# Kernel optimization log

Hardware: AMD Instinct MI355X
Metric: run time of the kernel (lower is better)

The kernel has to match this reference:

```python
import jax, jax.numpy as jnp
import numpy as np

N = 50000   # nodes
R = 4       # relation groups
E = 800000  # nnz per relation adjacency
ED = 200000 # decoded edges
H = 128     # hidden_dim
L = 64      # latent_dim
DH = 64     # decoder_hidden_dim


def setup_inputs() -> dict:
    key = jax.random.key(0)
    ks = iter(jax.random.split(key, 64))
    def nrm(shape, scale=1.0):
        return jax.random.normal(next(ks), shape, dtype=jnp.float32) * scale
    inp = {}
    inp["x_process"] = nrm((N, 62))
    inp["x_file"] = nrm((N, 37))
    inp["x_network"] = nrm((N, 37))
    def lin(prefix, din, dout):
        s = 1.0 / np.sqrt(din)
        inp[prefix + "_Ws"] = nrm((dout, din), s)
        inp[prefix + "_bs"] = nrm((dout,), s)
        inp[prefix + "_Wr"] = nrm((R, dout, din), s)
        inp[prefix + "_br"] = nrm((R, dout), s)
    lin("p1", 62, H); lin("p2", H, L)
    lin("f1", 37, H); lin("f2", H, L)
    lin("n1", 37, H); lin("n2", H, L)
    inp["gate_W"] = nrm((3, L), 1.0 / np.sqrt(L))
    inp["gate_b"] = nrm((3,), 0.1)
    inp["dec_W1"] = nrm((DH, 4 * L), 1.0 / np.sqrt(4 * L))
    inp["dec_b1"] = nrm((DH,), 0.1)
    inp["dec_W2"] = nrm((1, DH), 1.0 / np.sqrt(DH))
    inp["dec_b2"] = nrm((1,), 0.1)
    inp["adj_rows"] = jax.random.randint(next(ks), (R, E), 0, N, dtype=jnp.int32)
    inp["adj_cols"] = jax.random.randint(next(ks), (R, E), 0, N, dtype=jnp.int32)
    inp["adj_vals"] = jax.random.uniform(next(ks), (R, E), dtype=jnp.float32) * 0.1
    inp["edge_src"] = jax.random.randint(next(ks), (ED,), 0, N, dtype=jnp.int32)
    inp["edge_dst"] = jax.random.randint(next(ks), (ED,), 0, N, dtype=jnp.int32)
    return inp


def reference(x_process, x_file, x_network,
              p1_Ws, p1_bs, p1_Wr, p1_br, p2_Ws, p2_bs, p2_Wr, p2_br,
              f1_Ws, f1_bs, f1_Wr, f1_br, f2_Ws, f2_bs, f2_Wr, f2_br,
              n1_Ws, n1_bs, n1_Wr, n1_br, n2_Ws, n2_bs, n2_Wr, n2_br,
              gate_W, gate_b, dec_W1, dec_b1, dec_W2, dec_b2,
              adj_rows, adj_cols, adj_vals, edge_src, edge_dst):
    def spmm(rows, cols, vals, x):  # A @ x, A in COO: out[row] += val * x[col]
        return jax.ops.segment_sum(vals[:, None] * x[cols], rows, num_segments=N)

    def rgcn_layer(x, Ws, bs, Wr, br):
        out = x @ Ws.T + bs  # self_linear
        for r in range(R):
            out = out + spmm(adj_rows[r], adj_cols[r], adj_vals[r], x) @ Wr[r].T + br[r]
        return out / float(R + 1)

    def encoder(x, W1s, b1s, W1r, b1r, W2s, b2s, W2r, b2r):
        h = jax.nn.relu(rgcn_layer(x, W1s, b1s, W1r, b1r))
        # dropout p=0.0 / eval mode -> identity
        return rgcn_layer(h, W2s, b2s, W2r, b2r)

    z_p = encoder(x_process, p1_Ws, p1_bs, p1_Wr, p1_br, p2_Ws, p2_bs, p2_Wr, p2_br)
    z_f = encoder(x_file, f1_Ws, f1_bs, f1_Wr, f1_br, f2_Ws, f2_bs, f2_Wr, f2_br)
    z_n = encoder(x_network, n1_Ws, n1_bs, n1_Wr, n1_br, n2_Ws, n2_bs, n2_Wr, n2_br)

    # gated multi-view fusion: three Linear(latent,1) gates -> softmax over views
    scores = jnp.stack([z_p @ gate_W[0] + gate_b[0],
                        z_f @ gate_W[1] + gate_b[1],
                        z_n @ gate_W[2] + gate_b[2]], axis=1)  # [N, 3]
    alpha = jax.nn.softmax(scores, axis=1)
    z = alpha[:, 0:1] * z_p + alpha[:, 1:2] * z_f + alpha[:, 2:3] * z_n  # [N, L]

    # mlp edge decoder
    zs = z[edge_src]
    zd = z[edge_dst]
    feats = jnp.concatenate([zs, zd, zs * zd, jnp.abs(zs - zd)], axis=1)  # [ED, 4L]
    hid = jax.nn.relu(feats @ dec_W1.T + dec_b1)
    logits = (hid @ dec_W2.T + dec_b2)[:, 0]  # [ED]
    return logits
```

## Files before the change

kernel.cpp:

```cpp
#include <hip/hip_runtime.h>

#define N_NODES 50000
#define R_REL   4
#define E_NNZ   800000
#define ED_EDGES 200000
#define H_DIM   128
#define L_DIM   64

#define RN_TOTAL (R_REL * N_NODES)
#define ETOT     (R_REL * E_NNZ)

#define EPB   8192
#define NB    391
#define RBK   196
#define KBK   (R_REL * RBK)
#define HTOT  (KBK * NB)
#define SCB   300
#define MAXB  6144

#define WS_RP    0u
#define WS_HIST  800256u
#define WS_BSUM  2026496u
#define WS_CV    2030592u
#define WS_TMP   27630720u
#define WS_XALL  53230720u
#define WS_SP    72430720u
#define WS_SF    122030720u
#define WS_SN    151630720u
#define WS_HPR   181230720u
#define WS_HN    WS_TMP
#define WS_HF    WS_SP
#define WS_YSP   WS_XALL
#define WS_YSF   (WS_SP + 25600000u)
#define WS_YRP   WS_SF
#define WS_YRF   WS_SN
#define WS_YSN   WS_HPR
#define WS_YRN   WS_HF
#define WS_Z     194030720u

__device__ __forceinline__ ushort f2bf(float f) {
    unsigned u = __float_as_uint(f);
    unsigned r = (u + 0x7fffu + ((u >> 16) & 1u)) >> 16;
    return (ushort)r;
}
__device__ __forceinline__ float bf2f(ushort u) {
    return __uint_as_float(((unsigned)u) << 16);
}

__global__ void cast_xall_kernel(const float* __restrict__ xp, const float* __restrict__ xf,
                                 const float* __restrict__ xn, ushort* __restrict__ xall) {
    int i = blockIdx.x * 256 + threadIdx.x;
    if (i >= N_NODES * 192) return;
    int node = i / 192, k = i - node * 192;
    float v = 0.f;
    if (k < 62) v = xp[node * 62 + k];
    else if (k >= 64 && k < 138) {
        int j = k - 64, d = j >> 1;
        v = (j & 1) ? xn[node * 37 + d] : xf[node * 37 + d];
    }
    xall[i] = f2bf(v);
}

__global__ void radix_hist_kernel(const int* __restrict__ rows, int* __restrict__ H) {
    __shared__ int hist[KBK];
    int blk = blockIdx.x, t = threadIdx.x;
    for (int i = t; i < KBK; i += 256) hist[i] = 0;
    __syncthreads();
    int base = blk * EPB;
    #pragma unroll 1
    for (int i = 0; i < EPB / 256; i++) {
        int g = base + i * 256 + t;
        if (g < ETOT) {
            int r = g / E_NNZ;
            atomicAdd(&hist[r * RBK + (rows[g] >> 8)], 1);
        }
    }
    __syncthreads();
    for (int i = t; i < KBK; i += 256) H[i * NB + blk] = hist[i];
}

__global__ void scan_part_kernel(const int* __restrict__ H, int* __restrict__ bsum) {
    __shared__ int red[256];
    int base = blockIdx.x * 1024, t = threadIdx.x;
    int s = 0;
    #pragma unroll
    for (int i = 0; i < 4; i++) {
        int idx = base + i * 256 + t;
        if (idx < HTOT) s += H[idx];
    }
    red[t] = s; __syncthreads();
    for (int d = 128; d > 0; d >>= 1) {
        if (t < d) red[t] += red[t + d];
        __syncthreads();
    }
    if (t == 0) bsum[blockIdx.x] = red[0];
}

__global__ void scan_bsum_kernel(int* __restrict__ bsum, int* __restrict__ rp) {
    __shared__ int sh[512];
    int t = threadIdx.x;
    int v = (t < SCB) ? bsum[t] : 0;
    sh[t] = v; __syncthreads();
    for (int d = 1; d < 512; d <<= 1) {
        int u = (t >= d) ? sh[t - d] : 0;
        __syncthreads();
        sh[t] += u;
        __syncthreads();
    }
    if (t < SCB) bsum[t] = sh[t] - v;
    if (t == 0) rp[RN_TOTAL] = ETOT;
}

__global__ void scan_final_kernel(int* __restrict__ H, const int* __restrict__ bsum) {
    __shared__ int sh[256];
    int base = blockIdx.x * 1024, t = threadIdx.x;
    int c[4]; int s = 0;
    #pragma unroll
    for (int i = 0; i < 4; i++) {
        int idx = base + t * 4 + i;
        c[i] = (idx < HTOT) ? H[idx] : 0;
        s += c[i];
    }
    sh[t] = s; __syncthreads();
    for (int d = 1; d < 256; d <<= 1) {
        int u = (t >= d) ? sh[t - d] : 0;
        __syncthreads();
        sh[t] += u;
        __syncthreads();
    }
    int off = bsum[blockIdx.x] + sh[t] - s;
    #pragma unroll
    for (int i = 0; i < 4; i++) {
        int idx = base + t * 4 + i;
        if (idx < HTOT) H[idx] = off;
        off += c[i];
    }
}

__global__ void radix_scatter_kernel(const int* __restrict__ rows, const int* __restrict__ cols,
                                     const float* __restrict__ vals, const int* __restrict__ H,
                                     int2* __restrict__ tmp) {
    __shared__ int cur[KBK];
    int blk = blockIdx.x, t = threadIdx.x;
    for (int i = t; i < KBK; i += 256) cur[i] = H[i * NB + blk];
    __syncthreads();
    int base = blk * EPB;
    #pragma unroll 1
    for (int i = 0; i < EPB / 256; i++) {
        int g = base + i * 256 + t;
        if (g < ETOT) {
            int r = g / E_NNZ;
            int row = rows[g];
            int b = r * RBK + (row >> 8);
            int p = atomicAdd(&cur[b], 1);
            tmp[p] = make_int2(cols[g] | ((row & 255) << 16), __float_as_int(vals[g]));
        }
    }
}

__launch_bounds__(256)
__global__ void bucket_sort_kernel(const int2* __restrict__ tmp, const int* __restrict__ H,
                                   int* __restrict__ rp, int2* __restrict__ cse) {
    __shared__ int hist[256];
    __shared__ int sc[256];
    __shared__ int cur[256];
    __shared__ int2 eb[MAXB];
    int b = blockIdx.x, t = threadIdx.x;
    int start = H[b * NB];
    int end = (b == KBK - 1) ? ETOT : H[(b + 1) * NB];
    int cnt = end - start;
    bool useLds = (cnt <= MAXB);
    hist[t] = 0;
    __syncthreads();
    for (int i = t; i < cnt; i += 256) {
        int2 e = tmp[start + i];
        if (useLds) eb[i] = e;
        atomicAdd(&hist[(e.x >> 16) & 255], 1);
    }
    __syncthreads();
    sc[t] = hist[t]; __syncthreads();
    for (int d = 1; d < 256; d <<= 1) {
        int v = (t >= d) ? sc[t - d] : 0;
        __syncthreads();
        sc[t] += v;
        __syncthreads();
    }
    int pref = sc[t] - hist[t];
    int r = b / RBK, rh = b - r * RBK;
    int grow = rh * 256 + t;
    if (grow < N_NODES) rp[r * N_NODES + grow] = start + pref;
    cur[t] = start + pref;
    __syncthreads();
    for (int i = t; i < cnt; i += 256) {
        int2 e = useLds ? eb[i] : tmp[start + i];
        int rl = (e.x >> 16) & 255;
        int p = atomicAdd(&cur[rl], 1);
        cse[p] = make_int2(e.x & 0xFFFF, e.y);
    }
}

__global__ void spmm1_all_kernel(const ushort* __restrict__ xall,
                                 const int* __restrict__ rp, const int2* __restrict__ cse,
                                 float* __restrict__ Sp, float* __restrict__ Sf,
                                 float* __restrict__ Sn) {
    int wave = threadIdx.x >> 6, lane = threadIdx.x & 63;
    int row = blockIdx.x * 4 + wave;
    if (row >= N_NODES) return;
    bool lp = lane < 62, lf = lane < 37;
    int opx = lane;
    int ofn = 64 + 2 * lane;
    for (int r = 0; r < R_REL; r++) {
        int e0 = rp[r * N_NODES + row], e1 = rp[r * N_NODES + row + 1];
        float ap = 0.f, af = 0.f, an = 0.f;
        int e = e0;
        for (; e + 4 <= e1; e += 4) {
            int2 q0 = cse[e], q1 = cse[e + 1], q2 = cse[e + 2], q3 = cse[e + 3];
            const ushort* b0 = xall + (size_t)q0.x * 192;
            const ushort* b1 = xall + (size_t)q1.x * 192;
            const ushort* b2 = xall + (size_t)q2.x * 192;
            const ushort* b3 = xall + (size_t)q3.x * 192;
            ushort  p0 = b0[opx], p1 = b1[opx], p2 = b2[opx], p3 = b3[opx];
            ushort2 u0 = *(const ushort2*)&b0[ofn];
            ushort2 u1 = *(const ushort2*)&b1[ofn];
            ushort2 u2 = *(const ushort2*)&b2[ofn];
            ushort2 u3 = *(const ushort2*)&b3[ofn];
            float v0 = __int_as_float(q0.y), v1 = __int_as_float(q1.y);
            float v2 = __int_as_float(q2.y), v3 = __int_as_float(q3.y);
            ap += v0 * bf2f(p0) + v1 * bf2f(p1) + v2 * bf2f(p2) + v3 * bf2f(p3);
            af += v0 * bf2f(u0.x) + v1 * bf2f(u1.x) + v2 * bf2f(u2.x) + v3 * bf2f(u3.x);
            an += v0 * bf2f(u0.y) + v1 * bf2f(u1.y) + v2 * bf2f(u2.y) + v3 * bf2f(u3.y);
        }
        for (; e < e1; e++) {
            int2 q = cse[e];
            const ushort* b = xall + (size_t)q.x * 192;
            float v = __int_as_float(q.y);
            ap += v * bf2f(b[opx]);
            ushort2 u = *(const ushort2*)&b[ofn];
            af += v * bf2f(u.x);
            an += v * bf2f(u.y);
        }
        if (lp) Sp[row * 248 + r * 62 + lane] = ap;
        if (lf) { Sf[row * 148 + r * 37 + lane] = af; Sn[row * 148 + r * 37 + lane] = an; }
    }
}

__launch_bounds__(256)
__global__ void gemm1_kernel(const float* __restrict__ x, const float* __restrict__ S,
                             const float* __restrict__ Ws, const float* __restrict__ bs,
                             const float* __restrict__ Wr, const float* __restrict__ br,
                             float* __restrict__ h, int din) {
    __shared__ float sA[64 * 63];
    __shared__ float sW[62 * 132];
    int t = threadIdx.x;
    int i0 = blockIdx.x * 64;
    int rg = t >> 5, cg = t & 31;
    float acc[8][4] = {};
    for (int s = 0; s < 5; s++) {
        const float* Aptr; int astride;
        if (s == 0) { Aptr = x; astride = din; }
        else        { Aptr = S + (s - 1) * din; astride = 4 * din; }
        const float* Wp = (s == 0) ? Ws : (Wr + (s - 1) * H_DIM * din);
        __syncthreads();
        for (int idx = t; idx < 64 * din; idx += 256) {
            int rr = idx / din, k = idx - rr * din;
            int grow = i0 + rr;
            sA[rr * 63 + k] = (grow < N_NODES) ? Aptr[grow * astride + k] : 0.f;
        }
        for (int idx = t; idx < H_DIM * din; idx += 256) {
            int j = idx / din, k = idx - j * din;
            sW[k * 132 + j] = Wp[j * din + k];
        }
        __syncthreads();
        for (int k = 0; k < din; k++) {
            float a[8];
            #pragma unroll
            for (int rr = 0; rr < 8; rr++) a[rr] = sA[(rg * 8 + rr) * 63 + k];
            float4 w = *(const float4*)&sW[k * 132 + cg * 4];
            #pragma unroll
            for (int rr = 0; rr < 8; rr++) {
                acc[rr][0] += a[rr] * w.x; acc[rr][1] += a[rr] * w.y;
                acc[rr][2] += a[rr] * w.z; acc[rr][3] += a[rr] * w.w;
            }
        }
    }
    int j0 = cg * 4;
    float btot[4];
    #pragma unroll
    for (int cc = 0; cc < 4; cc++) {
        float b = bs[j0 + cc];
        #pragma unroll
        for (int r = 0; r < R_REL; r++) b += br[r * H_DIM + j0 + cc];
        btot[cc] = b;
    }
    #pragma unroll
    for (int rr = 0; rr < 8; rr++) {
        int grow = i0 + rg * 8 + rr;
        if (grow < N_NODES) {
            float4 o;
            o.x = fmaxf((acc[rr][0] + btot[0]) * 0.2f, 0.f);
            o.y = fmaxf((acc[rr][1] + btot[1]) * 0.2f, 0.f);
            o.z = fmaxf((acc[rr][2] + btot[2]) * 0.2f, 0.f);
            o.w = fmaxf((acc[rr][3] + btot[3]) * 0.2f, 0.f);
            *(float4*)&h[grow * H_DIM + j0] = o;
        }
    }
}

__launch_bounds__(256)
__global__ void gemm2_kernel(const float* __restrict__ h, const float* __restrict__ Ws2,
                             const float* __restrict__ Wr2, float* __restrict__ Yself,
                             ushort* __restrict__ Yrel) {
    __shared__ float sA[128 * 65];
    __shared__ float sW[64 * 68];
    int t = threadIdx.x;
    int i0 = blockIdx.x * 128;
    int ct = blockIdx.y;
    int rg = t >> 4, cg = t & 15;
    const float* Wp = (ct == 0) ? Ws2 : (Wr2 + (ct - 1) * 64 * H_DIM);
    float acc[8][4] = {};
    for (int kc = 0; kc < 2; kc++) {
        __syncthreads();
        for (int idx = t; idx < 128 * 64; idx += 256) {
            int rr = idx >> 6, k = idx & 63;
            int grow = i0 + rr;
            sA[rr * 65 + k] = (grow < N_NODES) ? h[grow * H_DIM + kc * 64 + k] : 0.f;
        }
        for (int idx = t; idx < 64 * 64; idx += 256) {
            int j = idx >> 6, k = idx & 63;
            sW[k * 68 + j] = Wp[j * H_DIM + kc * 64 + k];
        }
        __syncthreads();
        for (int k = 0; k < 64; k++) {
            float a[8];
            #pragma unroll
            for (int rr = 0; rr < 8; rr++) a[rr] = sA[(rg * 8 + rr) * 65 + k];
            float4 w = *(const float4*)&sW[k * 68 + cg * 4];
            #pragma unroll
            for (int rr = 0; rr < 8; rr++) {
                acc[rr][0] += a[rr] * w.x; acc[rr][1] += a[rr] * w.y;
                acc[rr][2] += a[rr] * w.z; acc[rr][3] += a[rr] * w.w;
            }
        }
    }
    #pragma unroll
    for (int rr = 0; rr < 8; rr++) {
        int grow = i0 + rg * 8 + rr;
        if (grow < N_NODES) {
            if (ct == 0) {
                float4 o = make_float4(acc[rr][0], acc[rr][1], acc[rr][2], acc[rr][3]);
                *(float4*)&Yself[(size_t)grow * 64 + cg * 4] = o;
            } else {
                ushort4 o;
                o.x = f2bf(acc[rr][0]); o.y = f2bf(acc[rr][1]);
                o.z = f2bf(acc[rr][2]); o.w = f2bf(acc[rr][3]);
                *(ushort4*)&Yrel[(size_t)grow * 256 + (ct - 1) * 64 + cg * 4] = o;
            }
        }
    }
}

__global__ void spmm2z_all_kernel(const float* __restrict__ Ysp, const ushort* __restrict__ Yrp,
                                  const float* __restrict__ Ysf, const ushort* __restrict__ Yrf,
                                  const float* __restrict__ Ysn, const ushort* __restrict__ Yrn,
                                  const int* __restrict__ rp, const int2* __restrict__ cse,
                                  const float* __restrict__ p_bs, const float* __restrict__ p_br,
                                  const float* __restrict__ f_bs, const float* __restrict__ f_br,
                                  const float* __restrict__ n_bs, const float* __restrict__ n_br,
                                  const float* __restrict__ gW, const float* __restrict__ gb,
                                  float* __restrict__ z) {
    int wave = threadIdx.x >> 6, lane = threadIdx.x & 63;
    int row = blockIdx.x * 4 + wave;
    if (row >= N_NODES) return;
    float aP = Ysp[(size_t)row * 64 + lane] + p_bs[lane]
             + p_br[lane] + p_br[64 + lane] + p_br[128 + lane] + p_br[192 + lane];
    float aF = Ysf[(size_t)row * 64 + lane] + f_bs[lane]
             + f_br[lane] + f_br[64 + lane] + f_br[128 + lane] + f_br[192 + lane];
    float aN = Ysn[(size_t)row * 64 + lane] + n_bs[lane]
             + n_br[lane] + n_br[64 + lane] + n_br[128 + lane] + n_br[192 + lane];
    for (int r = 0; r < R_REL; r++) {
        int e0 = rp[r * N_NODES + row], e1 = rp[r * N_NODES + row + 1];
        const ushort* yp = Yrp + r * 64 + lane;
        const ushort* yf = Yrf + r * 64 + lane;
        const ushort* yn = Yrn + r * 64 + lane;
        int e = e0;
        for (; e + 4 <= e1; e += 4) {
            int2 q0 = cse[e], q1 = cse[e + 1], q2 = cse[e + 2], q3 = cse[e + 3];
            size_t o0 = (size_t)q0.x * 256, o1 = (size_t)q1.x * 256;
            size_t o2 = (size_t)q2.x * 256, o3 = (size_t)q3.x * 256;
            float pp0 = bf2f(yp[o0]), pp1 = bf2f(yp[o1]), pp2 = bf2f(yp[o2]), pp3 = bf2f(yp[o3]);
            float ff0 = bf2f(yf[o0]), ff1 = bf2f(yf[o1]), ff2 = bf2f(yf[o2]), ff3 = bf2f(yf[o3]);
            float nn0 = bf2f(yn[o0]), nn1 = bf2f(yn[o1]), nn2 = bf2f(yn[o2]), nn3 = bf2f(yn[o3]);
            float v0 = __int_as_float(q0.y), v1 = __int_as_float(q1.y);
            float v2 = __int_as_float(q2.y), v3 = __int_as_float(q3.y);
            aP += v0 * pp0 + v1 * pp1 + v2 * pp2 + v3 * pp3;
            aF += v0 * ff0 + v1 * ff1 + v2 * ff2 + v3 * ff3;
            aN += v0 * nn0 + v1 * nn1 + v2 * nn2 + v3 * nn3;
        }
        for (; e < e1; e++) {
            int2 q = cse[e];
            size_t o = (size_t)q.x * 256;
            float v = __int_as_float(q.y);
            aP += v * bf2f(yp[o]);
            aF += v * bf2f(yf[o]);
            aN += v * bf2f(yn[o]);
        }
    }
    aP *= 0.2f; aF *= 0.2f; aN *= 0.2f;
    float sp = aP * gW[lane], sf = aF * gW[64 + lane], sn = aN * gW[128 + lane];
    #pragma unroll
    for (int d = 32; d >= 1; d >>= 1) {
        sp += __shfl_xor(sp, d);
        sf += __shfl_xor(sf, d);
        sn += __shfl_xor(sn, d);
    }
    sp += gb[0]; sf += gb[1]; sn += gb[2];
    float m = fmaxf(sp, fmaxf(sf, sn));
    float ep = __expf(sp - m), ef = __expf(sf - m), en = __expf(sn - m);
    float inv = 1.f / (ep + ef + en);
    z[row * 64 + lane] = (ep * aP + ef * aF + en * aN) * inv;
}

__launch_bounds__(256)
__global__ void decoder4_kernel(const float* __restrict__ z, const int* __restrict__ esrc,
                                const int* __restrict__ edst, const float* __restrict__ w1,
                                const float* __restrict__ b1, const float* __restrict__ w2,
                                const float* __restrict__ b2, float* __restrict__ out) {
    __shared__ float sW1[16384];
    int t = threadIdx.x;
    for (int i = t; i < 4096; i += 256)
        ((float4*)sW1)[i] = ((const float4*)w1)[i];
    __syncthreads();
    int e1 = blockIdx.x * 512 + t;
    int e2 = e1 + 256;
    bool v2 = e2 < ED_EDGES;
    if (e1 >= ED_EDGES) return;
    int s1 = esrc[e1], d1 = edst[e1];
    int s2 = v2 ? esrc[e2] : s1;
    int d2 = v2 ? edst[e2] : d1;
    const float4* zs1 = (const float4*)(z + (size_t)s1 * 64);
    const float4* zd1 = (const float4*)(z + (size_t)d1 * 64);
    const float4* zs2 = (const float4*)(z + (size_t)s2 * 64);
    const float4* zd2 = (const float4*)(z + (size_t)d2 * 64);
    float hid1[64], hid2[64];
    #pragma unroll
    for (int j = 0; j < 64; j++) { hid1[j] = 0.f; hid2[j] = 0.f; }
    #pragma unroll 1
    for (int kc = 0; kc < 16; kc++) {
        float4 a1 = zs1[kc], b1v4 = zd1[kc];
        float4 a2 = zs2[kc], b2v4 = zd2[kc];
        float4 p1, q1, p2, q2;
        p1.x = a1.x * b1v4.x; q1.x = fabsf(a1.x - b1v4.x);
        p1.y = a1.y * b1v4.y; q1.y = fabsf(a1.y - b1v4.y);
        p1.z = a1.z * b1v4.z; q1.z = fabsf(a1.z - b1v4.z);
        p1.w = a1.w * b1v4.w; q1.w = fabsf(a1.w - b1v4.w);
        p2.x = a2.x * b2v4.x; q2.x = fabsf(a2.x - b2v4.x);
        p2.y = a2.y * b2v4.y; q2.y = fabsf(a2.y - b2v4.y);
        p2.z = a2.z * b2v4.z; q2.z = fabsf(a2.z - b2v4.z);
        p2.w = a2.w * b2v4.w; q2.w = fabsf(a2.w - b2v4.w);
        const float* wb0 = sW1 + kc * 4;
        #pragma unroll
        for (int j = 0; j < 64; j++) {
            const float* wr = wb0 + j * 256;
            float4 wa = *(const float4*)(wr);
            float4 wbv = *(const float4*)(wr + 64);
            float4 wc = *(const float4*)(wr + 128);
            float4 wd = *(const float4*)(wr + 192);
            hid1[j] += a1.x * wa.x + a1.y * wa.y + a1.z * wa.z + a1.w * wa.w
                     + b1v4.x * wbv.x + b1v4.y * wbv.y + b1v4.z * wbv.z + b1v4.w * wbv.w
                     + p1.x * wc.x + p1.y * wc.y + p1.z * wc.z + p1.w * wc.w
                     + q1.x * wd.x + q1.y * wd.y + q1.z * wd.z + q1.w * wd.w;
            hid2[j] += a2.x * wa.x + a2.y * wa.y + a2.z * wa.z + a2.w * wa.w
                     + b2v4.x * wbv.x + b2v4.y * wbv.y + b2v4.z * wbv.z + b2v4.w * wbv.w
                     + p2.x * wc.x + p2.y * wc.y + p2.z * wc.z + p2.w * wc.w
                     + q2.x * wd.x + q2.y * wd.y + q2.z * wd.z + q2.w * wd.w;
        }
    }
    float lg1 = b2[0], lg2 = b2[0];
    #pragma unroll
    for (int j = 0; j < 64; j++) {
        float bj = b1[j], wj = w2[j];
        lg1 += fmaxf(hid1[j] + bj, 0.f) * wj;
        lg2 += fmaxf(hid2[j] + bj, 0.f) * wj;
    }
    out[e1] = lg1;
    if (v2) out[e2] = lg2;
}

extern "C" void kernel_launch(void* const* d_in, const int* in_sizes, int n_in,
                              void* d_out, int out_size, void* d_ws, size_t ws_size,
                              hipStream_t stream) {
    const float* x_p = (const float*)d_in[0];
    const float* x_f = (const float*)d_in[1];
    const float* x_n = (const float*)d_in[2];
    const float* p1_Ws = (const float*)d_in[3];  const float* p1_bs = (const float*)d_in[4];
    const float* p1_Wr = (const float*)d_in[5];  const float* p1_br = (const float*)d_in[6];
    const float* p2_Ws = (const float*)d_in[7];  const float* p2_bs = (const float*)d_in[8];
    const float* p2_Wr = (const float*)d_in[9];  const float* p2_br = (const float*)d_in[10];
    const float* f1_Ws = (const float*)d_in[11]; const float* f1_bs = (const float*)d_in[12];
    const float* f1_Wr = (const float*)d_in[13]; const float* f1_br = (const float*)d_in[14];
    const float* f2_Ws = (const float*)d_in[15]; const float* f2_bs = (const float*)d_in[16];
    const float* f2_Wr = (const float*)d_in[17]; const float* f2_br = (const float*)d_in[18];
    const float* n1_Ws = (const float*)d_in[19]; const float* n1_bs = (const float*)d_in[20];
    const float* n1_Wr = (const float*)d_in[21]; const float* n1_br = (const float*)d_in[22];
    const float* n2_Ws = (const float*)d_in[23]; const float* n2_bs = (const float*)d_in[24];
    const float* n2_Wr = (const float*)d_in[25]; const float* n2_br = (const float*)d_in[26];
    const float* gate_W = (const float*)d_in[27]; const float* gate_b = (const float*)d_in[28];
    const float* dec_W1 = (const float*)d_in[29]; const float* dec_b1 = (const float*)d_in[30];
    const float* dec_W2 = (const float*)d_in[31]; const float* dec_b2 = (const float*)d_in[32];
    const int*   adj_rows = (const int*)d_in[33];
    const int*   adj_cols = (const int*)d_in[34];
    const float* adj_vals = (const float*)d_in[35];
    const int*   edge_src = (const int*)d_in[36];
    const int*   edge_dst = (const int*)d_in[37];

    char* ws = (char*)d_ws;
    int*    rp   = (int*)(ws + WS_RP);
    int*    H    = (int*)(ws + WS_HIST);
    int*    bsum = (int*)(ws + WS_BSUM);
    int2*   cse  = (int2*)(ws + WS_CV);
    int2*   tmp  = (int2*)(ws + WS_TMP);
    ushort* xall = (ushort*)(ws + WS_XALL);
    float*  S_p = (float*)(ws + WS_SP);
    float*  S_f = (float*)(ws + WS_SF);
    float*  S_n = (float*)(ws + WS_SN);
    float*  h_p = (float*)(ws + WS_HPR);
    float*  h_f = (float*)(ws + WS_HF);
    float*  h_n = (float*)(ws + WS_HN);
    float*  Ys_p = (float*)(ws + WS_YSP);  ushort* Yr_p = (ushort*)(ws + WS_YRP);
    float*  Ys_f = (float*)(ws + WS_YSF);  ushort* Yr_f = (ushort*)(ws + WS_YRF);
    float*  Ys_n = (float*)(ws + WS_YSN);  ushort* Yr_n = (ushort*)(ws + WS_YRN);
    float*  z   = (float*)(ws + WS_Z);
    float*  out = (float*)d_out;

    cast_xall_kernel<<<(N_NODES * 192 + 255) / 256, 256, 0, stream>>>(x_p, x_f, x_n, xall);

    radix_hist_kernel<<<NB, 256, 0, stream>>>(adj_rows, H);
    scan_part_kernel<<<SCB, 256, 0, stream>>>(H, bsum);
    scan_bsum_kernel<<<1, 512, 0, stream>>>(bsum, rp);
    scan_final_kernel<<<SCB, 256, 0, stream>>>(H, bsum);
    radix_scatter_kernel<<<NB, 256, 0, stream>>>(adj_rows, adj_cols, adj_vals, H, tmp);
    bucket_sort_kernel<<<KBK, 256, 0, stream>>>(tmp, H, rp, cse);

    spmm1_all_kernel<<<N_NODES / 4, 256, 0, stream>>>(xall, rp, cse, S_p, S_f, S_n);

    int g1 = (N_NODES + 63) / 64;
    gemm1_kernel<<<g1, 256, 0, stream>>>(x_p, S_p, p1_Ws, p1_bs, p1_Wr, p1_br, h_p, 62);
    gemm1_kernel<<<g1, 256, 0, stream>>>(x_f, S_f, f1_Ws, f1_bs, f1_Wr, f1_br, h_f, 37);
    gemm1_kernel<<<g1, 256, 0, stream>>>(x_n, S_n, n1_Ws, n1_bs, n1_Wr, n1_br, h_n, 37);

    dim3 g2((N_NODES + 127) / 128, 5);
    gemm2_kernel<<<g2, 256, 0, stream>>>(h_p, p2_Ws, p2_Wr, Ys_p, Yr_p);
    gemm2_kernel<<<g2, 256, 0, stream>>>(h_f, f2_Ws, f2_Wr, Ys_f, Yr_f);
    gemm2_kernel<<<g2, 256, 0, stream>>>(h_n, n2_Ws, n2_Wr, Ys_n, Yr_n);

    spmm2z_all_kernel<<<N_NODES / 4, 256, 0, stream>>>(
        Ys_p, Yr_p, Ys_f, Yr_f, Ys_n, Yr_n, rp, cse,
        p2_bs, p2_br, f2_bs, f2_br, n2_bs, n2_br, gate_W, gate_b, z);

    decoder4_kernel<<<(ED_EDGES + 511) / 512, 256, 0, stream>>>(
        z, edge_src, edge_dst, dec_W1, dec_b1, dec_W2, dec_b2, out);
}
```

Baseline: 1.442 ms.

## Split edge decoder hidden units across two blocks and combine partial logits

The decoder kernel now splits the 64 hidden units into two halves along a second grid dimension, so each block holds half of W1 in shared memory and half the accumulators in registers. Each half writes a partial logit to workspace, and a small combine kernel sums the halves and adds the output bias. The aim is to double block count (the original launched only ~391 blocks) and lower register and LDS pressure for better occupancy. The cost is gathering z rows twice, an extra launch, and a partial-result round trip through memory.

```diff
diff --git a/kernel.cpp b/kernel.cpp
--- a/kernel.cpp
+++ b/kernel.cpp
@@ -37,6 +37,7 @@
 #define WS_YSN   WS_HPR
 #define WS_YRN   WS_HF
 #define WS_Z     194030720u
+#define WS_PART  WS_TMP
 
 __device__ __forceinline__ ushort f2bf(float f) {
     unsigned u = __float_as_uint(f);
@@ -421,14 +422,16 @@
 }
 
 __launch_bounds__(256)
-__global__ void decoder4_kernel(const float* __restrict__ z, const int* __restrict__ esrc,
+__global__ void decoder5_kernel(const float* __restrict__ z, const int* __restrict__ esrc,
                                 const int* __restrict__ edst, const float* __restrict__ w1,
                                 const float* __restrict__ b1, const float* __restrict__ w2,
-                                const float* __restrict__ b2, float* __restrict__ out) {
-    __shared__ float sW1[16384];
+                                float* __restrict__ part) {
+    __shared__ float sW1[8192];
     int t = threadIdx.x;
-    for (int i = t; i < 4096; i += 256)
-        ((float4*)sW1)[i] = ((const float4*)w1)[i];
+    int jh = blockIdx.y;
+    const float* w1h = w1 + jh * 32 * 256;
+    for (int i = t; i < 2048; i += 256)
+        ((float4*)sW1)[i] = ((const float4*)w1h)[i];
     __syncthreads();
     int e1 = blockIdx.x * 512 + t;
     int e2 = e1 + 256;
@@ -441,9 +444,9 @@
     const float4* zd1 = (const float4*)(z + (size_t)d1 * 64);
     const float4* zs2 = (const float4*)(z + (size_t)s2 * 64);
     const float4* zd2 = (const float4*)(z + (size_t)d2 * 64);
-    float hid1[64], hid2[64];
-    #pragma unroll
-    for (int j = 0; j < 64; j++) { hid1[j] = 0.f; hid2[j] = 0.f; }
+    float hid1[32], hid2[32];
+    #pragma unroll
+    for (int j = 0; j < 32; j++) { hid1[j] = 0.f; hid2[j] = 0.f; }
     #pragma unroll 1
     for (int kc = 0; kc < 16; kc++) {
         float4 a1 = zs1[kc], b1v4 = zd1[kc];
@@ -459,7 +462,7 @@
         p2.w = a2.w * b2v4.w; q2.w = fabsf(a2.w - b2v4.w);
         const float* wb0 = sW1 + kc * 4;
         #pragma unroll
-        for (int j = 0; j < 64; j++) {
+        for (int j = 0; j < 32; j++) {
             const float* wr = wb0 + j * 256;
             float4 wa = *(const float4*)(wr);
             float4 wbv = *(const float4*)(wr + 64);
@@ -475,15 +478,22 @@
                      + q2.x * wd.x + q2.y * wd.y + q2.z * wd.z + q2.w * wd.w;
         }
     }
-    float lg1 = b2[0], lg2 = b2[0];
-    #pragma unroll
-    for (int j = 0; j < 64; j++) {
-        float bj = b1[j], wj = w2[j];
+    float lg1 = 0.f, lg2 = 0.f;
+    #pragma unroll
+    for (int j = 0; j < 32; j++) {
+        int gj = jh * 32 + j;
+        float bj = b1[gj], wj = w2[gj];
         lg1 += fmaxf(hid1[j] + bj, 0.f) * wj;
         lg2 += fmaxf(hid2[j] + bj, 0.f) * wj;
     }
-    out[e1] = lg1;
-    if (v2) out[e2] = lg2;
+    part[(size_t)jh * ED_EDGES + e1] = lg1;
+    if (v2) part[(size_t)jh * ED_EDGES + e2] = lg2;
+}
+
+__global__ void dec_combine_kernel(const float* __restrict__ part, const float* __restrict__ b2,
+                                   float* __restrict__ out) {
+    int e = blockIdx.x * 256 + threadIdx.x;
+    if (e < ED_EDGES) out[e] = part[e] + part[ED_EDGES + e] + b2[0];
 }
 
 extern "C" void kernel_launch(void* const* d_in, const int* in_sizes, int n_in,
@@ -529,8 +539,9 @@
     float*  Ys_p = (float*)(ws + WS_YSP);  ushort* Yr_p = (ushort*)(ws + WS_YRP);
     float*  Ys_f = (float*)(ws + WS_YSF);  ushort* Yr_f = (ushort*)(ws + WS_YRF);
     float*  Ys_n = (float*)(ws + WS_YSN);  ushort* Yr_n = (ushort*)(ws + WS_YRN);
-    float*  z   = (float*)(ws + WS_Z);
-    float*  out = (float*)d_out;
+    float*  z    = (float*)(ws + WS_Z);
+    float*  part = (float*)(ws + WS_PART);
+    float*  out  = (float*)d_out;
 
     cast_xall_kernel<<<(N_NODES * 192 + 255) / 256, 256, 0, stream>>>(x_p, x_f, x_n, xall);
 
@@ -557,6 +568,8 @@
         Ys_p, Yr_p, Ys_f, Yr_f, Ys_n, Yr_n, rp, cse,
         p2_bs, p2_br, f2_bs, f2_br, n2_bs, n2_br, gate_W, gate_b, z);
 
-    decoder4_kernel<<<(ED_EDGES + 511) / 512, 256, 0, stream>>>(
-        z, edge_src, edge_dst, dec_W1, dec_b1, dec_W2, dec_b2, out);
-}
+    dim3 gd((ED_EDGES + 511) / 512, 2);
+    decoder5_kernel<<<gd, 256, 0, stream>>>(
+        z, edge_src, edge_dst, dec_W1, dec_b1, dec_W2, part);
+    dec_combine_kernel<<<(ED_EDGES + 255) / 256, 256, 0, stream>>>(part, dec_b2, out);
+}
```

Result: faster. 1.410 ms (-2.3%).
